# Kernel tuning notes

Hardware: AMD Instinct MI355X
Metric: run time of the kernel (lower is better)

The kernel has to match this reference:

```python
import jax, jax.numpy as jnp
import numpy as np

B, N, D, H, DEPTH = 2, 2048, 768, 12, 4
DH = D // H
SCALE = DH ** -0.5
EPS = 1e-5
FF = 4 * D


def layer_norm(x, w, b):
    m = jnp.mean(x, axis=-1, keepdims=True)
    v = jnp.mean((x - m) ** 2, axis=-1, keepdims=True)
    return (x - m) * jax.lax.rsqrt(v + EPS) * w + b


def to_heads(t):  # [b, n, D] -> [b, H, n, DH]
    b, n, _ = t.shape
    return t.reshape(b, n, H, DH).transpose(0, 2, 1, 3)


def merge_heads(t):  # [b, H, n, DH] -> [b, n, D]
    b, h, n, dh = t.shape
    return t.transpose(0, 2, 1, 3).reshape(b, n, D)


def attend(q, k, v, bias):
    s = jnp.einsum('bhid,bhjd->bhij', q, k) * SCALE + bias
    a = jax.nn.softmax(s, axis=-1)
    return merge_heads(jnp.einsum('bhij,bhjd->bhid', a, v))


def setup_inputs():
    key = jax.random.key(0)
    ks = iter(jax.random.split(key, 16))

    def p(shape, scale=0.02):
        return jax.random.normal(next(ks), shape, dtype=jnp.float32) * scale

    inp = {
        'x': jax.random.normal(next(ks), (B, N, D), dtype=jnp.float32),
        'context': jax.random.normal(next(ks), (B, N, D), dtype=jnp.float32),
        'relative_position_bias': jax.random.normal(next(ks), (1, H, N, N), dtype=jnp.float32) * 0.02,
        # self-attn params (stacked over depth)
        'ln1_w': jnp.ones((DEPTH, D), jnp.float32), 'ln1_b': jnp.zeros((DEPTH, D), jnp.float32),
        'w_qkv': p((DEPTH, D, 3 * D)),
        'w_so': p((DEPTH, D, D)), 'b_so': jnp.zeros((DEPTH, D), jnp.float32),
        # cross-attn params (shared LN applied to x and context, as in source)
        'ln2_w': jnp.ones((DEPTH, D), jnp.float32), 'ln2_b': jnp.zeros((DEPTH, D), jnp.float32),
        'w_q': p((DEPTH, D, D)), 'w_k': p((DEPTH, D, D)), 'w_v': p((DEPTH, D, D)),
        'w_co': p((DEPTH, D, D)), 'b_co': jnp.zeros((DEPTH, D), jnp.float32),
        # FFN params
        'ln3_w': jnp.ones((DEPTH, D), jnp.float32), 'ln3_b': jnp.zeros((DEPTH, D), jnp.float32),
        'w_f1': p((DEPTH, D, FF)), 'b_f1': jnp.zeros((DEPTH, FF), jnp.float32),
        'w_f2': p((DEPTH, FF, D)), 'b_f2': jnp.zeros((DEPTH, D), jnp.float32),
        # final norm
        'lnout_w': jnp.ones((D,), jnp.float32), 'lnout_b': jnp.zeros((D,), jnp.float32),
    }
    return inp


def reference(x, context, relative_position_bias,
              ln1_w, ln1_b, w_qkv, w_so, b_so,
              ln2_w, ln2_b, w_q, w_k, w_v, w_co, b_co,
              ln3_w, ln3_b, w_f1, b_f1, w_f2, b_f2,
              lnout_w, lnout_b):
    bias = relative_position_bias
    for i in range(DEPTH):
        # self-attention block (pre-norm, residual)
        xn = layer_norm(x, ln1_w[i], ln1_b[i])
        q, k, v = jnp.split(xn @ w_qkv[i], 3, axis=-1)
        o = attend(to_heads(q), to_heads(k), to_heads(v), bias)
        x = o @ w_so[i] + b_so[i] + x
        # cross-attention block (input_norm shared for x and context)
        xn = layer_norm(x, ln2_w[i], ln2_b[i])
        cn = layer_norm(context, ln2_w[i], ln2_b[i])
        o = attend(to_heads(xn @ w_q[i]), to_heads(cn @ w_k[i]), to_heads(cn @ w_v[i]), bias)
        x = o @ w_co[i] + b_co[i] + x
        # FFN block
        xn = layer_norm(x, ln3_w[i], ln3_b[i])
        h = jax.nn.gelu(xn @ w_f1[i] + b_f1[i], approximate=False)
        x = h @ w_f2[i] + b_f2[i] + x
    return layer_norm(x, lnout_w, lnout_b)
```

## Files before the change

### kernel.cpp

```cpp
#include <hip/hip_runtime.h>
#include <cstdint>
#include <cstddef>

#define DEV static __device__ __forceinline__

typedef float  f32x4 __attribute__((ext_vector_type(4)));
typedef float  f32x2 __attribute__((ext_vector_type(2)));
typedef short  s16x8 __attribute__((ext_vector_type(8)));
typedef unsigned short u16;
typedef unsigned int   u32;
typedef unsigned int   u32x4 __attribute__((ext_vector_type(4)));
typedef unsigned short u16x2 __attribute__((ext_vector_type(2)));
typedef unsigned short u16x4 __attribute__((ext_vector_type(4)));
typedef __bf16 bf16x8 __attribute__((ext_vector_type(8)));

#define LOG2E 1.4426950408889634f
#define QSCALE_CONST 0.18033688011112042f
#define BSCALE 256.0f
#define BINV   0.00390625f

DEV u16 f2bf(float f){ return __builtin_bit_cast(u16, (__bf16)f); }
DEV float bf2f(u16 v){ union { unsigned u; float f; } x; x.u = ((unsigned)v) << 16; return x.f; }

DEV float fexp2(float x){
#if __has_builtin(__builtin_amdgcn_exp2f)
  return __builtin_amdgcn_exp2f(x);
#else
  return exp2f(x);
#endif
}

DEV f32x4 mfma16(s16x8 a, s16x8 b, f32x4 c){
  return __builtin_amdgcn_mfma_f32_16x16x32_bf16(
      __builtin_bit_cast(bf16x8, a), __builtin_bit_cast(bf16x8, b), c, 0, 0, 0);
}

DEV void gld16(const void* g, void* l){
  __builtin_amdgcn_global_load_lds(
      (const __attribute__((address_space(1))) void*)(uintptr_t)g,
      (__attribute__((address_space(3))) void*)(unsigned)(uintptr_t)l,
      16, 0, 0);
}

#if __has_builtin(__builtin_amdgcn_cvt_pk_fp8_f32) && __has_builtin(__builtin_amdgcn_cvt_pk_f32_fp8)
DEV u32 pk4_fp8(f32x4 v){
  int r = __builtin_amdgcn_cvt_pk_fp8_f32(v[0], v[1], 0, false);
  r     = __builtin_amdgcn_cvt_pk_fp8_f32(v[2], v[3], r, true);
  return (u32)r;
}
template<bool HI>
DEV f32x2 upk_fp8(u32 w){
  return __builtin_amdgcn_cvt_pk_f32_fp8((int)w, HI);
}
#else
DEV unsigned enc1(float x){
  union{float f; unsigned u;} c; c.f = x;
  unsigned s = (c.u >> 24) & 0x80;
  int e = (int)((c.u >> 23) & 0xff) - 127;
  unsigned m = c.u & 0x7fffff;
  if (e >= -6){
    unsigned mant = m >> 20, rem = m & 0xfffff;
    if (rem > 0x80000 || (rem == 0x80000 && (mant & 1))) mant++;
    unsigned eb = (unsigned)(e + 7);
    if (mant == 8){ mant = 0; eb++; }
    if (eb >= 16){ eb = 15; mant = 6; }
    return s | (eb << 3) | mant;
  }
  if (e < -10) return s;
  int sh = -6 - e;
  unsigned full = (1u << 23) | m;
  unsigned mant = full >> (20 + sh);
  unsigned rem  = full & ((1u << (20 + sh)) - 1);
  unsigned half = 1u << (19 + sh);
  if (rem > half || (rem == half && (mant & 1))) mant++;
  if (mant == 8) return s | (1u << 3);
  return s | mant;
}
DEV u32 pk4_fp8(f32x4 v){
  return enc1(v[0]) | (enc1(v[1]) << 8) | (enc1(v[2]) << 16) | (enc1(v[3]) << 24);
}
DEV float dec1(unsigned b){
  int s = (b >> 7) & 1, e = (b >> 3) & 15; float m = (float)(b & 7) * 0.125f;
  float v = e ? ldexpf(1.0f + m, e - 7) : ldexpf(m, -6);
  return s ? -v : v;
}
template<bool HI>
DEV f32x2 upk_fp8(u32 w){
  unsigned lo = HI ? ((w >> 16) & 0xff) : (w & 0xff);
  unsigned h2 = HI ? ((w >> 24) & 0xff) : ((w >> 8) & 0xff);
  f32x2 r; r[0] = dec1(lo); r[1] = dec1(h2); return r;
}
#endif

__global__ void __launch_bounds__(256)
transpose_cvt(const float* __restrict__ src, u16* __restrict__ dst, int K, int N,
              size_t dzstride){
  int z = blockIdx.z;
  src += (size_t)z * K * N;
  dst += (size_t)z * dzstride;
  __shared__ float t[32][33];
  int n0 = blockIdx.x * 32, k0 = blockIdx.y * 32;
#pragma unroll
  for (int i = 0; i < 4; ++i)
    t[threadIdx.y + 8*i][threadIdx.x] = src[(size_t)(k0 + threadIdx.y + 8*i) * N + n0 + threadIdx.x];
  __syncthreads();
#pragma unroll
  for (int i = 0; i < 4; ++i)
    dst[(size_t)(n0 + threadIdx.y + 8*i) * K + k0 + threadIdx.x] = f2bf(t[threadIdx.x][threadIdx.y + 8*i]);
}

struct TPtrs { const float* src[20]; u16* dst[20]; };
__global__ void __launch_bounds__(256)
transpose_cvt_batch(TPtrs tp){
  const float* src = tp.src[blockIdx.z];
  u16* dst = tp.dst[blockIdx.z];
  __shared__ float t[32][33];
  int n0 = blockIdx.x * 32, k0 = blockIdx.y * 32;
#pragma unroll
  for (int i = 0; i < 4; ++i)
    t[threadIdx.y + 8*i][threadIdx.x] = src[(size_t)(k0 + threadIdx.y + 8*i) * 768 + n0 + threadIdx.x];
  __syncthreads();
#pragma unroll
  for (int i = 0; i < 4; ++i)
    dst[(size_t)(n0 + threadIdx.y + 8*i) * 768 + k0 + threadIdx.x] = f2bf(t[threadIdx.x][threadIdx.y + 8*i]);
}

__global__ void __launch_bounds__(256)
cvt_biasT(const float* __restrict__ in, unsigned char* __restrict__ out){
  const int kvt = blockIdx.x, qt = blockIdx.y, h = blockIdx.z, tid = threadIdx.x;
  const int q  = qt * 64 + ((tid >> 6) << 4) + (tid & 15);
  const int c0 = kvt * 64 + ((tid >> 4) & 3) * 4;
  const float* src = in + ((size_t)h * 2048 + q) * 2048;
  u32x4 wv;
#pragma unroll
  for (int mi = 0; mi < 4; ++mi){
    f32x4 v = *(const f32x4*)(src + c0 + mi * 16);
#pragma unroll
    for (int r = 0; r < 4; ++r) v[r] = fminf(fmaxf(v[r] * (LOG2E * BSCALE), -448.f), 448.f);
    wv[mi] = pk4_fp8(v);
  }
  *(u32x4*)(out + ((size_t)(h * 32 + qt) * 32 + kvt) * 4096 + tid * 16) = wv;
}

__global__ void __launch_bounds__(256)
lnv(const float* __restrict__ x, const float* __restrict__ w, const float* __restrict__ b,
    u16* __restrict__ out){
  const int wv = threadIdx.x >> 6, lane = threadIdx.x & 63;
  const float* wz = w + blockIdx.y * 768;
  const float* bz = b + blockIdx.y * 768;
  out += (size_t)blockIdx.y * 4096 * 768;
  const int row = blockIdx.x * 4 + wv;
  const float* xr = x + (size_t)row * 768;
  f32x4 t[3]; float s = 0.f, s2 = 0.f;
#pragma unroll
  for (int c = 0; c < 3; ++c){
    t[c] = *(const f32x4*)(xr + c * 256 + lane * 4);
#pragma unroll
    for (int j = 0; j < 4; ++j){ s += t[c][j]; s2 += t[c][j] * t[c][j]; }
  }
#pragma unroll
  for (int off = 1; off < 64; off <<= 1){ s += __shfl_xor(s, off); s2 += __shfl_xor(s2, off); }
  float m = s * (1.f/768.f);
  float rstd = rsqrtf(s2 * (1.f/768.f) - m * m + 1e-5f);
#pragma unroll
  for (int c = 0; c < 3; ++c){
    const int col = c * 256 + lane * 4;
    f32x4 wv4 = *(const f32x4*)(wz + col);
    f32x4 bv4 = *(const f32x4*)(bz + col);
    u16x4 o;
#pragma unroll
    for (int j = 0; j < 4; ++j) o[j] = f2bf((t[c][j] - m) * rstd * wv4[j] + bv4[j]);
    *(u16x4*)(out + (size_t)row * 768 + col) = o;
  }
}

template<typename OUT>
__global__ void __launch_bounds__(256)
red_ln(const u16* __restrict__ pb, const float* __restrict__ biasrow,
       float* __restrict__ xbuf, OUT* __restrict__ out,
       const float* __restrict__ lw, const float* __restrict__ lb){
  const int wv = threadIdx.x >> 6, lane = threadIdx.x & 63;
  const int row = blockIdx.x * 4 + wv;
  const size_t S = 4096ll * 768;
  const u16* p0 = pb + (size_t)row * 768;
  float* xr = xbuf + (size_t)row * 768;
  f32x4 t[3]; float s = 0.f, s2 = 0.f;
#pragma unroll
  for (int c = 0; c < 3; ++c){
    const int col = c * 256 + lane * 4;
    f32x4 v = *(const f32x4*)(biasrow + col);
    v += *(const f32x4*)(xr + col);
#pragma unroll
    for (int z = 0; z < 4; ++z){
      u16x4 pv = *(const u16x4*)(p0 + z * S + col);
#pragma unroll
      for (int j = 0; j < 4; ++j) v[j] += bf2f(pv[j]);
    }
    *(f32x4*)(xr + col) = v;
    t[c] = v;
#pragma unroll
    for (int j = 0; j < 4; ++j){ s += v[j]; s2 += v[j] * v[j]; }
  }
#pragma unroll
  for (int off = 1; off < 64; off <<= 1){ s += __shfl_xor(s, off); s2 += __shfl_xor(s2, off); }
  float m = s * (1.f/768.f);
  float rstd = rsqrtf(s2 * (1.f/768.f) - m * m + 1e-5f);
#pragma unroll
  for (int c = 0; c < 3; ++c){
    const int col = c * 256 + lane * 4;
    f32x4 wv4 = *(const f32x4*)(lw + col);
    f32x4 bv4 = *(const f32x4*)(lb + col);
    if constexpr (sizeof(OUT) == 2){
      u16x4 o;
#pragma unroll
      for (int j = 0; j < 4; ++j) o[j] = f2bf((t[c][j] - m) * rstd * wv4[j] + bv4[j]);
      *(u16x4*)((u16*)out + (size_t)row * 768 + col) = o;
    } else {
      f32x4 o;
#pragma unroll
      for (int j = 0; j < 4; ++j) o[j] = (t[c][j] - m) * rstd * wv4[j] + bv4[j];
      *(f32x4*)((float*)out + (size_t)row * 768 + col) = o;
    }
  }
}

template<int EPI>
__global__ void __launch_bounds__(256)
gemm_bf16(const u16* __restrict__ A, int lda, const u16* __restrict__ Bt, int ldb,
          int nk, u16* __restrict__ Cb, int ldc,
          const float* __restrict__ bias,
          const u16* __restrict__ A2, const u16* __restrict__ Bt2){
  __shared__ u16 As[2][128 * 32];
  __shared__ u16 Bs[2][128 * 32];
  float colscale = 1.0f;
  if constexpr (EPI == 4){
    const int z = blockIdx.z;
    if (z == 0){ colscale = QSCALE_CONST; }
    else { A = A2; Bt = Bt2 + (size_t)(z - 1) * 768 * 768; }
    Cb += z * 768;
  }
  if constexpr (EPI == 5){
    const int z = blockIdx.z;
    A  += (size_t)z * nk * 32;
    Bt += (size_t)z * nk * 32;
    Cb += (size_t)z * 4096 * 768;
  }
  const int gx = gridDim.x, nwg = gx * gridDim.y;
  int lin = blockIdx.y * gx + blockIdx.x;
  {
    const int qq = nwg >> 3, rr = nwg & 7;
    const int xc = lin & 7, oo = lin >> 3;
    lin = (xc < rr ? xc * (qq + 1) : rr * (qq + 1) + (xc - rr) * qq) + oo;
  }
  const int m0 = (lin % gx) * 128, n0 = (lin / gx) * 128;

  const int tid = threadIdx.x, w = tid >> 6, lane = tid & 63;
  const int l16 = lane & 15, g = lane >> 4;
  const int wm = (w >> 1) * 64, wn = (w & 1) * 64;
  f32x4 acc[4][4] = {};

  const u16* a0 = A  + (size_t)(m0 + (tid >> 2)) * lda + (tid & 3) * 8;
  const u16* a1 = A  + (size_t)(m0 + (tid >> 2) + 64) * lda + (tid & 3) * 8;
  const u16* b0 = Bt + (size_t)(n0 + (tid >> 2)) * ldb + (tid & 3) * 8;
  const u16* b1 = Bt + (size_t)(n0 + (tid >> 2) + 64) * ldb + (tid & 3) * 8;

  {
    char* ab = (char*)As[0]; char* bb = (char*)Bs[0];
    gld16(a0, ab + w * 1024); gld16(a1, ab + 4096 + w * 1024);
    gld16(b0, bb + w * 1024); gld16(b1, bb + 4096 + w * 1024);
  }
  __syncthreads();

  int cb = 0;
  for (int kt = 0; kt < nk; ++kt){
    if (kt + 1 < nk){
      const int k1 = (kt + 1) * 32;
      char* ab = (char*)As[cb ^ 1]; char* bb = (char*)Bs[cb ^ 1];
      gld16(a0 + k1, ab + w * 1024); gld16(a1 + k1, ab + 4096 + w * 1024);
      gld16(b0 + k1, bb + w * 1024); gld16(b1 + k1, bb + 4096 + w * 1024);
    }
    const u16* Ab = As[cb]; const u16* Bb = Bs[cb];
    s16x8 af[4], bfv[4];
#pragma unroll
    for (int mi = 0; mi < 4; ++mi)
      af[mi] = *(const s16x8*)(Ab + (wm + mi*16 + l16) * 32 + 8 * g);
#pragma unroll
    for (int ni = 0; ni < 4; ++ni)
      bfv[ni] = *(const s16x8*)(Bb + (wn + ni*16 + l16) * 32 + 8 * g);
#pragma unroll
    for (int mi = 0; mi < 4; ++mi)
#pragma unroll
      for (int ni = 0; ni < 4; ++ni)
        acc[mi][ni] = mfma16(af[mi], bfv[ni], acc[mi][ni]);
    __syncthreads();
    cb ^= 1;
  }

#pragma unroll
  for (int mi = 0; mi < 4; ++mi){
    const int rg = m0 + wm + mi*16 + 4*g;
#pragma unroll
    for (int ni = 0; ni < 4; ++ni){
      const int col = n0 + wn + ni*16 + l16;
      f32x4 v = acc[mi][ni];
#pragma unroll
      for (int r = 0; r < 4; ++r){
        const int row = rg + r;
        if constexpr (EPI == 2){
          float t = v[r] + bias[col];
          float ge = 0.5f * t * (1.0f + erff(t * 0.7071067811865476f));
          Cb[(size_t)row * ldc + col] = f2bf(ge);
        } else if constexpr (EPI == 3){
          float sc = (col < 768) ? QSCALE_CONST : 1.0f;
          Cb[(size_t)row * ldc + col] = f2bf(v[r] * sc);
        } else if constexpr (EPI == 4){
          Cb[(size_t)row * ldc + col] = f2bf(v[r] * colscale);
        } else {
          Cb[(size_t)row * 768 + col] = f2bf(v[r]);
        }
      }
    }
  }
}

__global__ void __launch_bounds__(256)
attn_kernel(const u16* __restrict__ qkv, const unsigned char* __restrict__ biasT,
            u16* __restrict__ out){
  __shared__ __align__(16) u16 Ks[2][4096];
  __shared__ __align__(16) u16 Vt[2][4096];
  __shared__ __align__(16) u16 Pl[4][1024];

  const int tid = threadIdx.x, w = tid >> 6, lane = tid & 63;
  const int l16 = lane & 15, g = lane >> 4;
  const int qt = blockIdx.x, h = blockIdx.y, b = blockIdx.z;
  const int rowbase = b * 2048, q0 = qt * 64;

  const int ci0 = w * 64 + lane, ci1 = ci0 + 256;
  const int r0 = ci0 >> 3, sc0 = ci0 & 7, r1 = ci1 >> 3, sc1 = ci1 & 7;
  const u16* kp0 = qkv + (size_t)(rowbase + r0) * 2304 + 768 + h * 64 + (((sc0 ^ (r0 & 7)) & 7) << 3);
  const u16* kp1 = qkv + (size_t)(rowbase + r1) * 2304 + 768 + h * 64 + (((sc1 ^ (r1 & 7)) & 7) << 3);
  const int dh0 = (tid & 31) * 2, vs = tid >> 5;
  const u16* vp = qkv + (size_t)(rowbase + vs * 8) * 2304 + 1536 + h * 64 + dh0;
  u16x2 vr[8];
  const unsigned char* bT = biasT + ((size_t)(h * 32 + qt) * 32) * 4096 + tid * 16;
  u32x4 brW, bnW;

  const u16* qrow = qkv + (size_t)(rowbase + q0 + w * 16 + l16) * 2304 + h * 64;
  s16x8 qf0 = *(const s16x8*)(qrow + 8 * g);
  s16x8 qf1 = *(const s16x8*)(qrow + 32 + 8 * g);

  f32x4 oacc[4] = {};
  float mrun = -3.0e38f, lrun = 0.f;
  const int sw = l16 & 7;

  {
    char* kb = (char*)Ks[0] + w * 1024;
    gld16(kp0, kb); gld16(kp1, kb + 4096);
#pragma unroll
    for (int i = 0; i < 8; ++i) vr[i] = *(const u16x2*)(vp + (size_t)i * 2304);
    brW = *(const u32x4*)(bT);
    s16x8 vA, vB;
#pragma unroll
    for (int j = 0; j < 8; ++j){ vA[j] = (short)vr[j][0]; vB[j] = (short)vr[j][1]; }
    *(s16x8*)(Vt[0] + dh0 * 64 + ((vs ^ (dh0 & 7)) << 3)) = vA;
    *(s16x8*)(Vt[0] + (dh0 + 1) * 64 + ((vs ^ ((dh0 + 1) & 7)) << 3)) = vB;
  }
  __syncthreads();

  for (int t = 0; t < 32; ++t){
    const int cb = t & 1;
    if (t < 31){
      const size_t koff = (size_t)(t + 1) * 64 * 2304;
      char* kb = (char*)Ks[cb ^ 1] + w * 1024;
      gld16(kp0 + koff, kb); gld16(kp1 + koff, kb + 4096);
      const u16* p = vp + koff;
#pragma unroll
      for (int i = 0; i < 8; ++i) vr[i] = *(const u16x2*)(p + (size_t)i * 2304);
      bnW = *(const u32x4*)(bT + (size_t)(t + 1) * 4096);
    }

    f32x4 st[4];
    __builtin_amdgcn_s_setprio(1);
#pragma unroll
    for (int mi = 0; mi < 4; ++mi){
      const int row = l16 + 16 * mi;
      s16x8 kf0 = *(const s16x8*)(Ks[cb] + row * 64 + ((g ^ sw) << 3));
      s16x8 kf1 = *(const s16x8*)(Ks[cb] + row * 64 + (((g + 4) ^ sw) << 3));
      f32x4 z = {};
      z = mfma16(kf0, qf0, z);
      st[mi] = mfma16(kf1, qf1, z);
    }
    __builtin_amdgcn_s_setprio(0);

    float tmax = -3.0e38f;
#pragma unroll
    for (int mi = 0; mi < 4; ++mi){
      f32x2 lo = upk_fp8<false>(brW[mi]);
      f32x2 hi = upk_fp8<true>(brW[mi]);
      st[mi][0] = fmaf(lo[0], BINV, st[mi][0]);
      st[mi][1] = fmaf(lo[1], BINV, st[mi][1]);
      st[mi][2] = fmaf(hi[0], BINV, st[mi][2]);
      st[mi][3] = fmaf(hi[1], BINV, st[mi][3]);
#pragma unroll
      for (int r = 0; r < 4; ++r) tmax = fmaxf(tmax, st[mi][r]);
    }
    tmax = fmaxf(tmax, __shfl_xor(tmax, 16));
    tmax = fmaxf(tmax, __shfl_xor(tmax, 32));
    if (!__all(tmax <= mrun + 8.f)){
      float mnew = fmaxf(mrun, tmax);
      float al = fexp2(mrun - mnew);
      mrun = mnew;
      lrun *= al;
#pragma unroll
      for (int r = 0; r < 4; ++r){
        float aq = __shfl(al, 4 * g + r);
#pragma unroll
        for (int ni = 0; ni < 4; ++ni) oacc[ni][r] *= aq;
      }
    }
    float ssum = 0.f;
#pragma unroll
    for (int mi = 0; mi < 4; ++mi){
      u16x4 pk;
#pragma unroll
      for (int r = 0; r < 4; ++r){
        float pv = fexp2(st[mi][r] - mrun);
        ssum += pv;
        pk[r] = f2bf(pv);
      }
      *(u16x4*)(Pl[w] + l16 * 64 + (((2*mi + (g >> 1)) ^ sw) << 3) + 4 * (g & 1)) = pk;
    }
    ssum += __shfl_xor(ssum, 16);
    ssum += __shfl_xor(ssum, 32);
    lrun += ssum;

    __builtin_amdgcn_s_setprio(1);
#pragma unroll
    for (int ks2 = 0; ks2 < 2; ++ks2){
      s16x8 pf = *(const s16x8*)(Pl[w] + l16 * 64 + (((4*ks2 + g) ^ sw) << 3));
#pragma unroll
      for (int ni = 0; ni < 4; ++ni){
        const int dh = l16 + 16 * ni;
        s16x8 vf = *(const s16x8*)(Vt[cb] + dh * 64 + (((4*ks2 + g) ^ sw) << 3));
        oacc[ni] = mfma16(pf, vf, oacc[ni]);
      }
    }
    __builtin_amdgcn_s_setprio(0);

    if (t < 31){
      s16x8 vA, vB;
#pragma unroll
      for (int j = 0; j < 8; ++j){ vA[j] = (short)vr[j][0]; vB[j] = (short)vr[j][1]; }
      *(s16x8*)(Vt[cb ^ 1] + dh0 * 64 + ((vs ^ (dh0 & 7)) << 3)) = vA;
      *(s16x8*)(Vt[cb ^ 1] + (dh0 + 1) * 64 + ((vs ^ ((dh0 + 1) & 7)) << 3)) = vB;
      brW = bnW;
    }
    __syncthreads();
  }

#pragma unroll
  for (int r = 0; r < 4; ++r){
    float lq = __shfl(lrun, 4 * g + r);
    float inv = 1.0f / lq;
    const int row = rowbase + q0 + w * 16 + 4 * g + r;
#pragma unroll
    for (int ni = 0; ni < 4; ++ni)
      out[(size_t)row * 768 + h * 64 + l16 + 16 * ni] = f2bf(oacc[ni][r] * inv);
  }
}

extern "C" void kernel_launch(void* const* d_in, const int* in_sizes, int n_in,
                              void* d_out, int out_size, void* d_ws, size_t ws_size,
                              hipStream_t stream){
  const float* in_x    = (const float*)d_in[0];
  const float* in_ctx  = (const float*)d_in[1];
  const float* in_bias = (const float*)d_in[2];
  const float* ln1_w = (const float*)d_in[3];
  const float* ln1_b = (const float*)d_in[4];
  const float* w_qkv = (const float*)d_in[5];
  const float* w_so  = (const float*)d_in[6];
  const float* b_so  = (const float*)d_in[7];
  const float* ln2_w = (const float*)d_in[8];
  const float* ln2_b = (const float*)d_in[9];
  const float* w_q   = (const float*)d_in[10];
  const float* w_k   = (const float*)d_in[11];
  const float* w_v   = (const float*)d_in[12];
  const float* w_co  = (const float*)d_in[13];
  const float* b_co  = (const float*)d_in[14];
  const float* ln3_w = (const float*)d_in[15];
  const float* ln3_b = (const float*)d_in[16];
  const float* w_f1  = (const float*)d_in[17];
  const float* b_f1  = (const float*)d_in[18];
  const float* w_f2  = (const float*)d_in[19];
  const float* b_f2  = (const float*)d_in[20];
  const float* lnout_w = (const float*)d_in[21];
  const float* lnout_b = (const float*)d_in[22];

  char* p = (char*)d_ws;
  float* xbuf  = (float*)p;  p += 4096ll * 768 * 4;
  u16* pbuf    = (u16*)p;    p += 4ll * 4096 * 768 * 2;
  u16* xn      = (u16*)p;    p += 4096ll * 768 * 2;
  u16* cn      = (u16*)p;    p += 4ll * 4096 * 768 * 2;
  u16* qkvb    = (u16*)p;    p += 4096ll * 2304 * 2;
  u16* attO    = (u16*)p;    p += 4096ll * 768 * 2;
  u16* ffh     = (u16*)p;    p += 4096ll * 3072 * 2;
  u16* wqkvT   = (u16*)p;    p += 4ll * 2304 * 768 * 2;
  u16* wsoT    = (u16*)p;    p += 4ll * 768 * 768 * 2;
  u16* wqT     = (u16*)p;    p += 4ll * 768 * 768 * 2;
  u16* wkvT    = (u16*)p;    p += 4ll * 1536 * 768 * 2;
  u16* wcoT    = (u16*)p;    p += 4ll * 768 * 768 * 2;
  u16* wf1T    = (u16*)p;    p += 4ll * 3072 * 768 * 2;
  u16* wf2T    = (u16*)p;    p += 4ll * 768 * 3072 * 2;
  unsigned char* biasT = (unsigned char*)p; p += 12ll * 2048 * 2048;

  hipMemcpyAsync(xbuf, in_x, 4096ll * 768 * 4, hipMemcpyDeviceToDevice, stream);

  const dim3 tb(32, 8);
  transpose_cvt<<<dim3(72, 24, 4), tb, 0, stream>>>(w_qkv, wqkvT, 768, 2304, 2304ll*768);
  transpose_cvt<<<dim3(96, 24, 4), tb, 0, stream>>>(w_f1,  wf1T,  768, 3072, 3072ll*768);
  transpose_cvt<<<dim3(24, 96, 4), tb, 0, stream>>>(w_f2,  wf2T,  3072, 768, 768ll*3072);
  {
    TPtrs tp;
    for (int i = 0; i < 4; ++i){
      tp.src[i*5+0] = w_so + (size_t)i*768*768;  tp.dst[i*5+0] = wsoT + (size_t)i*768*768;
      tp.src[i*5+1] = w_q  + (size_t)i*768*768;  tp.dst[i*5+1] = wqT  + (size_t)i*768*768;
      tp.src[i*5+2] = w_k  + (size_t)i*768*768;  tp.dst[i*5+2] = wkvT + (size_t)i*1536*768;
      tp.src[i*5+3] = w_v  + (size_t)i*768*768;  tp.dst[i*5+3] = wkvT + (size_t)i*1536*768 + 768ll*768;
      tp.src[i*5+4] = w_co + (size_t)i*768*768;  tp.dst[i*5+4] = wcoT + (size_t)i*768*768;
    }
    transpose_cvt_batch<<<dim3(24, 24, 20), tb, 0, stream>>>(tp);
  }
  cvt_biasT<<<dim3(32, 32, 12), 256, 0, stream>>>(in_bias, biasT);
  lnv<<<dim3(1024, 4), 256, 0, stream>>>(in_ctx, ln2_w, ln2_b, cn);
  lnv<<<dim3(1024, 1), 256, 0, stream>>>(xbuf, ln1_w, ln1_b, xn);

  const dim3 ag(32, 12, 2);
  for (int i = 0; i < 4; ++i){
    gemm_bf16<3><<<dim3(32, 18), 256, 0, stream>>>(xn, 768, wqkvT + (size_t)i*2304*768, 768, 24,
                                                   qkvb, 2304, nullptr, nullptr, nullptr);
    attn_kernel<<<ag, 256, 0, stream>>>(qkvb, biasT, attO);
    gemm_bf16<5><<<dim3(32, 6, 4), 256, 0, stream>>>(attO, 768, wsoT + (size_t)i*768*768, 768, 6,
                                                     pbuf, 768, nullptr, nullptr, nullptr);
    red_ln<u16><<<1024, 256, 0, stream>>>(pbuf, b_so + i*768, xbuf, xn, ln2_w + i*768, ln2_b + i*768);
    gemm_bf16<4><<<dim3(32, 6, 3), 256, 0, stream>>>(xn, 768, wqT + (size_t)i*768*768, 768, 24,
                                                     qkvb, 2304, nullptr,
                                                     cn + (size_t)i*4096*768, wkvT + (size_t)i*1536*768);
    attn_kernel<<<ag, 256, 0, stream>>>(qkvb, biasT, attO);
    gemm_bf16<5><<<dim3(32, 6, 4), 256, 0, stream>>>(attO, 768, wcoT + (size_t)i*768*768, 768, 6,
                                                     pbuf, 768, nullptr, nullptr, nullptr);
    red_ln<u16><<<1024, 256, 0, stream>>>(pbuf, b_co + i*768, xbuf, xn, ln3_w + i*768, ln3_b + i*768);
    gemm_bf16<2><<<dim3(32, 24), 256, 0, stream>>>(xn, 768, wf1T + (size_t)i*3072*768, 768, 24,
                                                   ffh, 3072, b_f1 + i*3072, nullptr, nullptr);
    gemm_bf16<5><<<dim3(32, 6, 4), 256, 0, stream>>>(ffh, 3072, wf2T + (size_t)i*768*3072, 3072, 24,
                                                     pbuf, 768, nullptr, nullptr, nullptr);
    if (i < 3)
      red_ln<u16><<<1024, 256, 0, stream>>>(pbuf, b_f2 + i*768, xbuf, xn, ln1_w + (i+1)*768, ln1_b + (i+1)*768);
    else
      red_ln<float><<<1024, 256, 0, stream>>>(pbuf, b_f2 + i*768, xbuf, (float*)d_out, lnout_w, lnout_b);
  }
}
```

Baseline: 1.313 ms.

## Store residual stream in bf16 and halve split-K for output projections

The fp32 residual buffer becomes bf16. A new ln_init kernel converts the input and produces the first layernorm, which replaces the device-to-device copy. The attention output-projection GEMMs now use a split-K of 2 instead of 4, and red_ln is templated on the split count so it reads fewer partial buffers. This cuts memory traffic in the reduction and LN kernels, but rounding the residual stream to bf16 after every block costs accuracy.

Result: faster. 1.273 ms (-3.0%).

```diff
diff --git a/kernel.cpp b/kernel.cpp
--- a/kernel.cpp
+++ b/kernel.cpp
@@ -174,29 +174,67 @@
   }
 }
 
-template<typename OUT>
+__global__ void __launch_bounds__(256)
+ln_init(const float* __restrict__ x, const float* __restrict__ w, const float* __restrict__ b,
+        u16* __restrict__ xn, u16* __restrict__ xbuf){
+  const int wv = threadIdx.x >> 6, lane = threadIdx.x & 63;
+  const int row = blockIdx.x * 4 + wv;
+  const float* xr = x + (size_t)row * 768;
+  f32x4 t[3]; float s = 0.f, s2 = 0.f;
+#pragma unroll
+  for (int c = 0; c < 3; ++c){
+    t[c] = *(const f32x4*)(xr + c * 256 + lane * 4);
+#pragma unroll
+    for (int j = 0; j < 4; ++j){ s += t[c][j]; s2 += t[c][j] * t[c][j]; }
+  }
+#pragma unroll
+  for (int off = 1; off < 64; off <<= 1){ s += __shfl_xor(s, off); s2 += __shfl_xor(s2, off); }
+  float m = s * (1.f/768.f);
+  float rstd = rsqrtf(s2 * (1.f/768.f) - m * m + 1e-5f);
+#pragma unroll
+  for (int c = 0; c < 3; ++c){
+    const int col = c * 256 + lane * 4;
+    f32x4 wv4 = *(const f32x4*)(w + col);
+    f32x4 bv4 = *(const f32x4*)(b + col);
+    u16x4 o, xb;
+#pragma unroll
+    for (int j = 0; j < 4; ++j){
+      o[j]  = f2bf((t[c][j] - m) * rstd * wv4[j] + bv4[j]);
+      xb[j] = f2bf(t[c][j]);
+    }
+    *(u16x4*)(xn   + (size_t)row * 768 + col) = o;
+    *(u16x4*)(xbuf + (size_t)row * 768 + col) = xb;
+  }
+}
+
+template<typename OUT, int NZ>
 __global__ void __launch_bounds__(256)
 red_ln(const u16* __restrict__ pb, const float* __restrict__ biasrow,
-       float* __restrict__ xbuf, OUT* __restrict__ out,
+       u16* __restrict__ xbuf, OUT* __restrict__ out,
        const float* __restrict__ lw, const float* __restrict__ lb){
   const int wv = threadIdx.x >> 6, lane = threadIdx.x & 63;
   const int row = blockIdx.x * 4 + wv;
   const size_t S = 4096ll * 768;
   const u16* p0 = pb + (size_t)row * 768;
-  float* xr = xbuf + (size_t)row * 768;
+  u16* xr = xbuf + (size_t)row * 768;
   f32x4 t[3]; float s = 0.f, s2 = 0.f;
 #pragma unroll
   for (int c = 0; c < 3; ++c){
     const int col = c * 256 + lane * 4;
     f32x4 v = *(const f32x4*)(biasrow + col);
-    v += *(const f32x4*)(xr + col);
-#pragma unroll
-    for (int z = 0; z < 4; ++z){
+    u16x4 xv = *(const u16x4*)(xr + col);
+#pragma unroll
+    for (int j = 0; j < 4; ++j) v[j] += bf2f(xv[j]);
+#pragma unroll
+    for (int z = 0; z < NZ; ++z){
       u16x4 pv = *(const u16x4*)(p0 + z * S + col);
 #pragma unroll
       for (int j = 0; j < 4; ++j) v[j] += bf2f(pv[j]);
     }
-    *(f32x4*)(xr + col) = v;
+    u16x4 xo;
+#pragma unroll
+    for (int j = 0; j < 4; ++j) xo[j] = f2bf(v[j]);
+    *(u16x4*)(xr + col) = xo;
     t[c] = v;
 #pragma unroll
     for (int j = 0; j < 4; ++j){ s += v[j]; s2 += v[j] * v[j]; }
@@ -497,7 +535,7 @@
   const float* lnout_b = (const float*)d_in[22];
 
   char* p = (char*)d_ws;
-  float* xbuf  = (float*)p;  p += 4096ll * 768 * 4;
+  u16* xbuf    = (u16*)p;    p += 4096ll * 768 * 2;
   u16* pbuf    = (u16*)p;    p += 4ll * 4096 * 768 * 2;
   u16* xn      = (u16*)p;    p += 4096ll * 768 * 2;
   u16* cn      = (u16*)p;    p += 4ll * 4096 * 768 * 2;
@@ -513,8 +551,6 @@
   u16* wf2T    = (u16*)p;    p += 4ll * 768 * 3072 * 2;
   unsigned char* biasT = (unsigned char*)p; p += 12ll * 2048 * 2048;
 
-  hipMemcpyAsync(xbuf, in_x, 4096ll * 768 * 4, hipMemcpyDeviceToDevice, stream);
-
   const dim3 tb(32, 8);
   transpose_cvt<<<dim3(72, 24, 4), tb, 0, stream>>>(w_qkv, wqkvT, 768, 2304, 2304ll*768);
   transpose_cvt<<<dim3(96, 24, 4), tb, 0, stream>>>(w_f1,  wf1T,  768, 3072, 3072ll*768);
@@ -532,30 +568,30 @@
   }
   cvt_biasT<<<dim3(32, 32, 12), 256, 0, stream>>>(in_bias, biasT);
   lnv<<<dim3(1024, 4), 256, 0, stream>>>(in_ctx, ln2_w, ln2_b, cn);
-  lnv<<<dim3(1024, 1), 256, 0, stream>>>(xbuf, ln1_w, ln1_b, xn);
+  ln_init<<<1024, 256, 0, stream>>>(in_x, ln1_w, ln1_b, xn, xbuf);
 
   const dim3 ag(32, 12, 2);
   for (int i = 0; i < 4; ++i){
     gemm_bf16<3><<<dim3(32, 18), 256, 0, stream>>>(xn, 768, wqkvT + (size_t)i*2304*768, 768, 24,
                                                    qkvb, 2304, nullptr, nullptr, nullptr);
     attn_kernel<<<ag, 256, 0, stream>>>(qkvb, biasT, attO);
-    gemm_bf16<5><<<dim3(32, 6, 4), 256, 0, stream>>>(attO, 768, wsoT + (size_t)i*768*768, 768, 6,
+    gemm_bf16<5><<<dim3(32, 6, 2), 256, 0, stream>>>(attO, 768, wsoT + (size_t)i*768*768, 768, 12,
                                                      pbuf, 768, nullptr, nullptr, nullptr);
-    red_ln<u16><<<1024, 256, 0, stream>>>(pbuf, b_so + i*768, xbuf, xn, ln2_w + i*768, ln2_b + i*768);
+    red_ln<u16,2><<<1024, 256, 0, stream>>>(pbuf, b_so + i*768, xbuf, xn, ln2_w + i*768, ln2_b + i*768);
     gemm_bf16<4><<<dim3(32, 6, 3), 256, 0, stream>>>(xn, 768, wqT + (size_t)i*768*768, 768, 24,
                                                      qkvb, 2304, nullptr,
                                                      cn + (size_t)i*4096*768, wkvT + (size_t)i*1536*768);
     attn_kernel<<<ag, 256, 0, stream>>>(qkvb, biasT, attO);
-    gemm_bf16<5><<<dim3(32, 6, 4), 256, 0, stream>>>(attO, 768, wcoT + (size_t)i*768*768, 768, 6,
+    gemm_bf16<5><<<dim3(32, 6, 2), 256, 0, stream>>>(attO, 768, wcoT + (size_t)i*768*768, 768, 12,
                                                      pbuf, 768, nullptr, nullptr, nullptr);
-    red_ln<u16><<<1024, 256, 0, stream>>>(pbuf, b_co + i*768, xbuf, xn, ln3_w + i*768, ln3_b + i*768);
+    red_ln<u16,2><<<1024, 256, 0, stream>>>(pbuf, b_co + i*768, xbuf, xn, ln3_w + i*768, ln3_b + i*768);
     gemm_bf16<2><<<dim3(32, 24), 256, 0, stream>>>(xn, 768, wf1T + (size_t)i*3072*768, 768, 24,
                                                    ffh, 3072, b_f1 + i*3072, nullptr, nullptr);
     gemm_bf16<5><<<dim3(32, 6, 4), 256, 0, stream>>>(ffh, 3072, wf2T + (size_t)i*768*3072, 3072, 24,
                                                      pbuf, 768, nullptr, nullptr, nullptr);
     if (i < 3)
-      red_ln<u16><<<1024, 256, 0, stream>>>(pbuf, b_f2 + i*768, xbuf, xn, ln1_w + (i+1)*768, ln1_b + (i+1)*768);
+      red_ln<u16,4><<<1024, 256, 0, stream>>>(pbuf, b_f2 + i*768, xbuf, xn, ln1_w + (i+1)*768, ln1_b + (i+1)*768);
     else
-      red_ln<float><<<1024, 256, 0, stream>>>(pbuf, b_f2 + i*768, xbuf, (float*)d_out, lnout_w, lnout_b);
-  }
-}
+      red_ln<float,4><<<1024, 256, 0, stream>>>(pbuf, b_f2 + i*768, xbuf, (float*)d_out, lnout_w, lnout_b);
+  }
+}
```
